# Performance work log

Measured on AMD Instinct MI355X. Metric: run time of the kernel, lower is better.

The kernel has to match this reference:

```python
import jax, jax.numpy as jnp
import numpy as np

N = 100000
F_IN = 128
HID = 8
HEADS = 8
CLASSES = 40
NEG_SLOPE = 0.2


def gat_conv(x, src, dst, W, a_src, a_dst, bias, heads, out_c):
    # x: [N, F]; W: [F, heads*out_c]; a_src/a_dst: [heads, out_c]; bias: [heads*out_c]
    n = x.shape[0]
    h = (x @ W).reshape(n, heads, out_c)                       # [N, H, C]
    al_src = jnp.sum(h * a_src, axis=-1)                       # [N, H]
    al_dst = jnp.sum(h * a_dst, axis=-1)                       # [N, H]
    e = jax.nn.leaky_relu(al_src[src] + al_dst[dst], NEG_SLOPE)  # [E, H]
    # segment softmax over destination node (PyG softmax over edge_index[1])
    m = jax.ops.segment_max(e, dst, num_segments=n)            # [N, H]
    m = jnp.where(jnp.isfinite(m), m, 0.0)
    ex = jnp.exp(e - m[dst])
    denom = jax.ops.segment_sum(ex, dst, num_segments=n)       # [N, H]
    alpha = ex / denom[dst]                                    # [E, H]
    msg = h[src] * alpha[:, :, None]                           # [E, H, C]
    out = jax.ops.segment_sum(msg, dst, num_segments=n)        # [N, H, C]
    return out.reshape(n, heads * out_c) + bias


def setup_inputs() -> dict:
    key = jax.random.key(0)
    ks = jax.random.split(key, 12)
    E = 1600000
    x = jax.random.normal(ks[0], (N, F_IN), dtype=jnp.float32)
    edge_index = jax.random.randint(ks[1], (2, E), 0, N, dtype=jnp.int32)
    # layer 1: in=F_IN, out=HID, heads=HEADS, concat -> 64 channels
    s1 = 1.0 / np.sqrt(F_IN)
    W1 = jax.random.uniform(ks[2], (F_IN, HEADS * HID), jnp.float32, -s1, s1)
    a_src1 = jax.random.uniform(ks[3], (HEADS, HID), jnp.float32, -0.3, 0.3)
    a_dst1 = jax.random.uniform(ks[4], (HEADS, HID), jnp.float32, -0.3, 0.3)
    b1 = jnp.zeros((HEADS * HID,), jnp.float32)
    # layer 2: in=64, out=CLASSES, heads=1
    d2 = HEADS * HID
    s2 = 1.0 / np.sqrt(d2)
    W2 = jax.random.uniform(ks[5], (d2, CLASSES), jnp.float32, -s2, s2)
    a_src2 = jax.random.uniform(ks[6], (1, CLASSES), jnp.float32, -0.3, 0.3)
    a_dst2 = jax.random.uniform(ks[7], (1, CLASSES), jnp.float32, -0.3, 0.3)
    b2 = jnp.zeros((CLASSES,), jnp.float32)
    return {"x": x, "edge_index": edge_index, "W1": W1, "a_src1": a_src1,
            "a_dst1": a_dst1, "b1": b1, "W2": W2, "a_src2": a_src2,
            "a_dst2": a_dst2, "b2": b2}


def reference(x, edge_index, W1, a_src1, a_dst1, b1, W2, a_src2, a_dst2, b2):
    # PyG GATConv adds self-loops by default
    loops = jnp.arange(N, dtype=edge_index.dtype)
    src = jnp.concatenate([edge_index[0], loops])
    dst = jnp.concatenate([edge_index[1], loops])
    h = gat_conv(x, src, dst, W1, a_src1, a_dst1, b1, HEADS, HID)
    h = jax.nn.relu(h)  # dropout is identity in eval mode
    out = gat_conv(h, src, dst, W2, a_src2, a_dst2, b2, 1, CLASSES)
    return jax.nn.log_softmax(out, axis=1)
```

## Files before the change

kernel.cpp:

```cpp
#include <hip/hip_runtime.h>
#include <hip/hip_bf16.h>
#include <math.h>

#define FIN 128
#define HID 8
#define HEADS 8
#define C1 64
#define CLS 40
#define NSLOPE 0.2f
#define NINF (-__builtin_inff())

typedef __hip_bfloat16 bf16;
typedef unsigned int uint32;
typedef int vint4 __attribute__((ext_vector_type(4)));

__device__ __forceinline__ float lrelu(float x) { return x >= 0.f ? x : NSLOPE * x; }
__device__ __forceinline__ vint4 ldnt4(const int* p) {
    return __builtin_nontemporal_load((const vint4*)p);
}
__device__ __forceinline__ float bfLO(uint32 u) { return __uint_as_float(u << 16); }
__device__ __forceinline__ float bfHI(uint32 u) { return __uint_as_float(u & 0xffff0000u); }
__device__ __forceinline__ uint32 packbf(float a, float b) {
    union { bf16 h[2]; uint32 u; } p;
    p.h[0] = __float2bfloat16(a); p.h[1] = __float2bfloat16(b);
    return p.u;
}

__global__ __launch_bounds__(256) void k_scan1(const int* __restrict__ deg,
    int* __restrict__ rowstart, int* __restrict__ bsum, int n) {
    __shared__ int sm[256];
    int t = threadIdx.x, i = blockIdx.x * 256 + t;
    int v = (i < n) ? deg[i] + 1 : 0;
    sm[t] = v; __syncthreads();
    int x = v;
    for (int off = 1; off < 256; off <<= 1) {
        int tv = (t >= off) ? sm[t - off] : 0;
        __syncthreads();
        x += tv; sm[t] = x; __syncthreads();
    }
    if (i < n) rowstart[i] = x - v;
    if (t == 255) bsum[blockIdx.x] = x;
}

__global__ __launch_bounds__(512) void k_scan2(int* __restrict__ bsum, int nb) {
    __shared__ int sm[512];
    int t = threadIdx.x;
    int v = (t < nb) ? bsum[t] : 0;
    sm[t] = v; __syncthreads();
    int x = v;
    for (int off = 1; off < 512; off <<= 1) {
        int tv = (t >= off) ? sm[t - off] : 0;
        __syncthreads();
        x += tv; sm[t] = x; __syncthreads();
    }
    if (t < nb) bsum[t] = x - v;
}

__global__ void k_scan3(int* __restrict__ rowstart, const int* __restrict__ bsum,
                        int n, int total) {
    int i = blockIdx.x * blockDim.x + threadIdx.x;
    if (i < n) rowstart[i] += bsum[i >> 8];
    if (i == 0) rowstart[n] = total;
}

__global__ __launch_bounds__(256) void k_scatter(const int* __restrict__ ei,
    int E, int En, int n, int* __restrict__ rowcur, int* __restrict__ csr) {
    int g = blockIdx.x & 7;
    int per8 = (n + 7) >> 3;
    int lo = g * per8, hi = min(n, lo + per8);
    int idx = (blockIdx.x >> 3) * 256 + threadIdx.x;
    int e0 = idx * 4;
    if (e0 + 3 < E) {
        vint4 dv = ldnt4(ei + E + e0);
        vint4 sv = ldnt4(ei + e0);
        if (dv.x >= lo && dv.x < hi) csr[atomicAdd(&rowcur[dv.x], 1)] = sv.x;
        if (dv.y >= lo && dv.y < hi) csr[atomicAdd(&rowcur[dv.y], 1)] = sv.y;
        if (dv.z >= lo && dv.z < hi) csr[atomicAdd(&rowcur[dv.z], 1)] = sv.z;
        if (dv.w >= lo && dv.w < hi) csr[atomicAdd(&rowcur[dv.w], 1)] = sv.w;
    } else {
        int e_end = min(e0 + 4, En);
        for (int e = e0; e < e_end; ++e) {
            int s, d;
            if (e < E) { s = ei[e]; d = ei[E + e]; } else { s = d = e - E; }
            if (d >= lo && d < hi) csr[atomicAdd(&rowcur[d], 1)] = s;
        }
    }
}

__global__ __launch_bounds__(256) void gemm1_kernel(
    const float* __restrict__ x, const float* __restrict__ W1,
    const float* __restrict__ a_src, const float* __restrict__ a_dst,
    bf16* __restrict__ h1b, float* __restrict__ alS, float* __restrict__ alD,
    int n, const int* __restrict__ ei, int E, int* __restrict__ deg) {
    __shared__ uint32 Wlu[FIN][C1 / 2];
    __shared__ float xs[64][FIN + 4];
    int t = threadIdx.x;
    const float4* W4 = (const float4*)W1;
    for (int i = t; i < FIN * (C1 / 4); i += 256) {
        float4 w = W4[i];
        int row = i / (C1 / 4), c4 = i % (C1 / 4);
        Wlu[row][c4 * 2]     = packbf(w.x, w.y);
        Wlu[row][c4 * 2 + 1] = packbf(w.z, w.w);
    }
    int node0 = blockIdx.x * 64;
    for (int i = t; i < 64 * (FIN / 4); i += 256) {
        int r = i / (FIN / 4), c = i % (FIN / 4);
        int nn = node0 + r;
        float4 v = {0.f, 0.f, 0.f, 0.f};
        if (nn < n) v = ((const float4*)x)[(size_t)nn * (FIN / 4) + c];
        *(float4*)&xs[r][c * 4] = v;
    }
    __syncthreads();
    int cg = t & 15, ng = t >> 4;
    int head = cg >> 1, hc = (cg & 1) * 4;
    float acc[4][4];
    #pragma unroll
    for (int i = 0; i < 4; ++i)
        for (int j = 0; j < 4; ++j) acc[i][j] = 0.f;
    #pragma unroll 2
    for (int k = 0; k < FIN; ++k) {
        uint2 wu = *(const uint2*)&Wlu[k][cg * 2];
        float w0 = bfLO(wu.x), w1 = bfHI(wu.x);
        float w2 = bfLO(wu.y), w3 = bfHI(wu.y);
        #pragma unroll
        for (int i = 0; i < 4; ++i) {
            float xv = xs[ng * 4 + i][k];
            acc[i][0] += xv * w0; acc[i][1] += xv * w1;
            acc[i][2] += xv * w2; acc[i][3] += xv * w3;
        }
    }
    float a_s[4], a_d[4];
    #pragma unroll
    for (int j = 0; j < 4; ++j) {
        a_s[j] = a_src[head * HID + hc + j];
        a_d[j] = a_dst[head * HID + hc + j];
    }
    #pragma unroll
    for (int i = 0; i < 4; ++i) {
        int node = node0 + ng * 4 + i;
        float as = acc[i][0] * a_s[0] + acc[i][1] * a_s[1]
                 + acc[i][2] * a_s[2] + acc[i][3] * a_s[3];
        float ad = acc[i][0] * a_d[0] + acc[i][1] * a_d[1]
                 + acc[i][2] * a_d[2] + acc[i][3] * a_d[3];
        as += __shfl_xor(as, 1, 64);
        ad += __shfl_xor(ad, 1, 64);
        if (node < n) {
            union { ushort4 u; bf16 b[4]; } pk;
            #pragma unroll
            for (int j = 0; j < 4; ++j) pk.b[j] = __float2bfloat16(acc[i][j]);
            ((ushort4*)h1b)[(size_t)node * (C1 / 4) + cg] = pk.u;
            if ((cg & 1) == 0) {
                alS[node * HEADS + head] = as;
                alD[node * HEADS + head] = ad;
            }
        }
    }
    int g = blockIdx.x * 256 + t;
    int gstride = gridDim.x * 256;
    int nI4 = E >> 2;
    for (int idx = g; idx < nI4; idx += gstride) {
        vint4 dv = ldnt4(ei + E + idx * 4);
        atomicAdd(&deg[dv.x], 1); atomicAdd(&deg[dv.y], 1);
        atomicAdd(&deg[dv.z], 1); atomicAdd(&deg[dv.w], 1);
    }
    if (g == 0)
        for (int e = nI4 * 4; e < E; ++e) atomicAdd(&deg[ei[E + e]], 1);
}

__global__ __launch_bounds__(256) void k_agg1(
    const int* __restrict__ csr, const int* __restrict__ rowend,
    const int* __restrict__ deg,
    const float* __restrict__ alS, const float* __restrict__ alD,
    const bf16* __restrict__ h1b, const float* __restrict__ b1,
    const float* __restrict__ W2, const float* __restrict__ aS2,
    const float* __restrict__ aD2,
    bf16* __restrict__ h2b, float* __restrict__ alS2, float* __restrict__ alD2,
    int n) {
    __shared__ int    ls[4][64];
    __shared__ float4 lp4[4][128];
    __shared__ float  xrow[4][64];
    __shared__ float  Wl[C1][CLS];
    int t = threadIdx.x;
    for (int i = t; i < C1 * CLS; i += 256) Wl[i / CLS][i % CLS] = W2[i];
    __syncthreads();
    int lane = t & 63, wv = t >> 6;
    int c32 = lane & 31;
    int par = lane >> 5;
    int hp  = c32 >> 2;
    const float* lpf = (const float*)&lp4[wv][0];
    const uint32* h1u = (const uint32*)h1b;
    int stride = gridDim.x * 4;

    for (int d = blockIdx.x * 4 + wv; d < n; d += stride) {
        float4 ad0 = *(const float4*)(alD + d * HEADS);
        float4 ad1 = *(const float4*)(alD + d * HEADS + 4);
        float adh[8] = {ad0.x, ad0.y, ad0.z, ad0.w, ad1.x, ad1.y, ad1.z, ad1.w};
        int cnt  = deg[d] + 1;
        int base = rowend[d] - cnt;
        float accx = 0.f, accy = 0.f, den = 0.f;
        for (int jb = 0; jb < cnt; jb += 64) {
            int ec = min(64, cnt - jb);
            int jj = jb + lane;
            bool on = jj < cnt;
            int s = on ? csr[base + jj] : 0;
            ls[wv][lane] = s;
            float4 a0 = *(const float4*)(alS + s * HEADS);
            float4 a1 = *(const float4*)(alS + s * HEADS + 4);
            float av[8] = {a0.x, a0.y, a0.z, a0.w, a1.x, a1.y, a1.z, a1.w};
            float pv[8];
            #pragma unroll
            for (int h = 0; h < 8; ++h)
                pv[h] = on ? __expf(lrelu(av[h] + adh[h])) : 0.f;
            lp4[wv][lane * 2]     = make_float4(pv[0], pv[1], pv[2], pv[3]);
            lp4[wv][lane * 2 + 1] = make_float4(pv[4], pv[5], pv[6], pv[7]);
            int j = 0;
            for (; j + 8 <= ec; j += 8) {
                int j0 = j + par, j1 = j + 2 + par, j2 = j + 4 + par, j3 = j + 6 + par;
                int s0 = ls[wv][j0], s1 = ls[wv][j1];
                int s2 = ls[wv][j2], s3 = ls[wv][j3];
                float p0 = lpf[j0 * 8 + hp], p1 = lpf[j1 * 8 + hp];
                float p2 = lpf[j2 * 8 + hp], p3 = lpf[j3 * 8 + hp];
                uint32 u0 = h1u[s0 * 32 + c32], u1 = h1u[s1 * 32 + c32];
                uint32 u2 = h1u[s2 * 32 + c32], u3 = h1u[s3 * 32 + c32];
                accx = fmaf(p0, bfLO(u0), accx); accy = fmaf(p0, bfHI(u0), accy);
                accx = fmaf(p1, bfLO(u1), accx); accy = fmaf(p1, bfHI(u1), accy);
                accx = fmaf(p2, bfLO(u2), accx); accy = fmaf(p2, bfHI(u2), accy);
                accx = fmaf(p3, bfLO(u3), accx); accy = fmaf(p3, bfHI(u3), accy);
                den += p0 + p1 + p2 + p3;
            }
            for (; j < ec; j += 2) {
                int j0 = j + par;
                int s0 = ls[wv][j0];
                float p0 = lpf[j0 * 8 + hp];
                uint32 u0 = h1u[s0 * 32 + c32];
                accx = fmaf(p0, bfLO(u0), accx);
                accy = fmaf(p0, bfHI(u0), accy);
                den += p0;
            }
        }
        accx += __shfl_xor(accx, 32, 64);
        accy += __shfl_xor(accy, 32, 64);
        den  += __shfl_xor(den, 32, 64);
        if (lane < 32) {
            float2 bb = *(const float2*)(b1 + 2 * c32);
            float vx = accx / den + bb.x;
            float vy = accy / den + bb.y;
            vx = vx > 0.f ? vx : 0.f;
            vy = vy > 0.f ? vy : 0.f;
            *(float2*)&xrow[wv][2 * c32] = make_float2(vx, vy);
        }
        bool act = lane < CLS;
        float h2c = 0.f;
        if (act) {
            #pragma unroll 8
            for (int k = 0; k < C1; ++k) h2c = fmaf(xrow[wv][k], Wl[k][lane], h2c);
        }
        float as2 = act ? h2c * aS2[lane] : 0.f;
        float ad2 = act ? h2c * aD2[lane] : 0.f;
        #pragma unroll
        for (int off = 1; off < 64; off <<= 1) {
            as2 += __shfl_xor(as2, off, 64);
            ad2 += __shfl_xor(ad2, off, 64);
        }
        if (act) h2b[d * CLS + lane] = __float2bfloat16(h2c);
        if (lane == 0) { alS2[d] = as2; alD2[d] = ad2; }
    }
}

__global__ __launch_bounds__(256) void k_agg2(
    const int* __restrict__ csr, const int* __restrict__ rowend,
    const int* __restrict__ deg,
    const float* __restrict__ alS, const float* __restrict__ alD,
    const bf16* __restrict__ h2b, const float* __restrict__ b2,
    float* __restrict__ out, int n) {
    __shared__ int2 lsp[4][64];
    int lane = threadIdx.x & 63, wv = threadIdx.x >> 6;
    int d = blockIdx.x * 4 + wv;
    if (d >= n) return;
    int c32 = lane & 31;
    int par = lane >> 5;
    bool actB = c32 < (CLS / 2);
    const uint32* h2u = (const uint32*)h2b;
    float ad = alD[d];
    int cnt  = deg[d] + 1;
    int base = rowend[d] - cnt;
    float accx = 0.f, accy = 0.f, den = 0.f;
    for (int jb = 0; jb < cnt; jb += 64) {
        int ec = min(64, cnt - jb);
        int jj = jb + lane;
        bool on = jj < cnt;
        int s = on ? csr[base + jj] : 0;
        float p = on ? __expf(lrelu(alS[s] + ad)) : 0.f;
        den += p;
        lsp[wv][lane] = make_int2(s, __float_as_int(p));
        if (actB) {
            int j = 0;
            for (; j + 8 <= ec; j += 8) {
                int2 e0 = lsp[wv][j + par],     e1 = lsp[wv][j + 2 + par];
                int2 e2 = lsp[wv][j + 4 + par], e3 = lsp[wv][j + 6 + par];
                uint32 u0 = h2u[e0.x * 20 + c32], u1 = h2u[e1.x * 20 + c32];
                uint32 u2 = h2u[e2.x * 20 + c32], u3 = h2u[e3.x * 20 + c32];
                float p0 = __int_as_float(e0.y), p1 = __int_as_float(e1.y);
                float p2 = __int_as_float(e2.y), p3 = __int_as_float(e3.y);
                accx = fmaf(p0, bfLO(u0), accx); accy = fmaf(p0, bfHI(u0), accy);
                accx = fmaf(p1, bfLO(u1), accx); accy = fmaf(p1, bfHI(u1), accy);
                accx = fmaf(p2, bfLO(u2), accx); accy = fmaf(p2, bfHI(u2), accy);
                accx = fmaf(p3, bfLO(u3), accx); accy = fmaf(p3, bfHI(u3), accy);
            }
            for (; j < ec; j += 2) {
                int2 e0 = lsp[wv][j + par];
                uint32 u0 = h2u[e0.x * 20 + c32];
                float p0 = __int_as_float(e0.y);
                accx = fmaf(p0, bfLO(u0), accx);
                accy = fmaf(p0, bfHI(u0), accy);
            }
        }
    }
    #pragma unroll
    for (int off = 1; off < 64; off <<= 1) den += __shfl_xor(den, off, 64);
    accx += __shfl_xor(accx, 32, 64);
    accy += __shfl_xor(accy, 32, 64);
    bool owner = (lane < 32) && actB;
    float vx = 0.f, vy = 0.f;
    if (owner) {
        float2 bb = *(const float2*)(b2 + 2 * c32);
        vx = accx / den + bb.x;
        vy = accy / den + bb.y;
    }
    float mx = owner ? fmaxf(vx, vy) : NINF;
    #pragma unroll
    for (int off = 1; off < 64; off <<= 1) mx = fmaxf(mx, __shfl_xor(mx, off, 64));
    float sum = owner ? (__expf(vx - mx) + __expf(vy - mx)) : 0.f;
    #pragma unroll
    for (int off = 1; off < 64; off <<= 1) sum += __shfl_xor(sum, off, 64);
    float lse = mx + __logf(sum);
    if (owner)
        *(float2*)(out + (size_t)d * CLS + 2 * c32) = make_float2(vx - lse, vy - lse);
}

extern "C" void kernel_launch(void* const* d_in, const int* in_sizes, int n_in,
                              void* d_out, int out_size, void* d_ws, size_t ws_size,
                              hipStream_t stream) {
    const float* x   = (const float*)d_in[0];
    const int*   ei  = (const int*)d_in[1];
    const float* W1  = (const float*)d_in[2];
    const float* aS1 = (const float*)d_in[3];
    const float* aD1 = (const float*)d_in[4];
    const float* b1  = (const float*)d_in[5];
    const float* W2  = (const float*)d_in[6];
    const float* aS2 = (const float*)d_in[7];
    const float* aD2 = (const float*)d_in[8];
    const float* b2  = (const float*)d_in[9];
    float* out = (float*)d_out;

    int n = in_sizes[0] / FIN;
    int E = in_sizes[1] / 2;
    int En = E + n;

    char* wsb = (char*)d_ws;
    bf16*  h1b  = (bf16*)wsb;
    bf16*  h2b  = h1b + (size_t)n * C1;
    float* alS1 = (float*)(h2b + (size_t)n * CLS);
    float* alD1 = alS1 + (size_t)n * HEADS;
    float* alS2 = alD1 + (size_t)n * HEADS;
    float* alD2 = alS2 + n;
    int*   csr  = (int*)(alD2 + n);
    int*   rowstart = csr + En;
    int*   deg  = rowstart + n + 1;
    int*   bsum = deg + n;

    const int T = 256;
    int nb = (n + 255) / 256;

    (void)hipMemsetAsync(deg, 0, (size_t)n * sizeof(int), stream);
    gemm1_kernel<<<(n + 63) / 64, T, 0, stream>>>(x, W1, aS1, aD1, h1b, alS1, alD1,
                                                  n, ei, E, deg);

    k_scan1<<<nb, T, 0, stream>>>(deg, rowstart, bsum, n);
    k_scan2<<<1, 512, 0, stream>>>(bsum, nb);
    k_scan3<<<nb, T, 0, stream>>>(rowstart, bsum, n, En);
    int chunks = (En + 1023) / 1024;
    k_scatter<<<chunks * 8, T, 0, stream>>>(ei, E, En, n, rowstart, csr);

    k_agg1<<<2048, T, 0, stream>>>(csr, rowstart, deg, alS1, alD1, h1b, b1,
                                   W2, aS2, aD2, h2b, alS2, alD2, n);

    k_agg2<<<(n + 3) / 4, T, 0, stream>>>(csr, rowstart, deg, alS2, alD2, h2b, b2, out, n);
}
```

Before: 330.2 us.

## Compute in-degree via per-block LDS histograms over node slices

Replaces the global atomic degree counting, which did one global atomic per edge across all gemm1 blocks, with a sliced LDS histogram. 256 blocks each own one of 16 node slices and scan a sixteenth of the edges, counting into shared memory. They then flush nonzero bins to global with one atomic per bin. The goal is to cut global atomic contention and traffic. In exchange each block reads its edge share and discards most entries, since only about 1/16 fall in its slice. The flush still issues many global atomics, and the shared buffer must be large enough for about 6250 ints.

```diff
diff --git a/kernel.cpp b/kernel.cpp
--- a/kernel.cpp
+++ b/kernel.cpp
@@ -155,16 +155,31 @@
             }
         }
     }
-    int g = blockIdx.x * 256 + t;
-    int gstride = gridDim.x * 256;
-    int nI4 = E >> 2;
-    for (int idx = g; idx < nI4; idx += gstride) {
-        vint4 dv = ldnt4(ei + E + idx * 4);
-        atomicAdd(&deg[dv.x], 1); atomicAdd(&deg[dv.y], 1);
-        atomicAdd(&deg[dv.z], 1); atomicAdd(&deg[dv.w], 1);
-    }
-    if (g == 0)
-        for (int e = nI4 * 4; e < E; ++e) atomicAdd(&deg[ei[E + e]], 1);
+    if (blockIdx.x < 256) {
+        __syncthreads();
+        int* hist = (int*)&xs[0][0];
+        int SLICE = (n + 15) >> 4;
+        int sl = blockIdx.x & 15;
+        int lo = sl * SLICE, hi = min(n, lo + SLICE);
+        int nbin = hi - lo;
+        for (int i = t; i < nbin; i += 256) hist[i] = 0;
+        __syncthreads();
+        int nI4 = E >> 2;
+        for (int idx = (blockIdx.x >> 4) * 256 + t; idx < nI4; idx += 4096) {
+            vint4 dv = ldnt4(ei + E + idx * 4);
+            if (dv.x >= lo && dv.x < hi) atomicAdd(&hist[dv.x - lo], 1);
+            if (dv.y >= lo && dv.y < hi) atomicAdd(&hist[dv.y - lo], 1);
+            if (dv.z >= lo && dv.z < hi) atomicAdd(&hist[dv.z - lo], 1);
+            if (dv.w >= lo && dv.w < hi) atomicAdd(&hist[dv.w - lo], 1);
+        }
+        if (blockIdx.x == 0)
+            for (int e = nI4 * 4 + t; e < E; e += 256) atomicAdd(&deg[ei[E + e]], 1);
+        __syncthreads();
+        for (int i = t; i < nbin; i += 256) {
+            int v = hist[i];
+            if (v) atomicAdd(&deg[lo + i], v);
+        }
+    }
 }
 
 __global__ __launch_bounds__(256) void k_agg1(
@@ -371,10 +386,12 @@
 
     const int T = 256;
     int nb = (n + 255) / 256;
+    int nblocks = (n + 63) / 64;
+    if (nblocks < 256) nblocks = 256;
 
     (void)hipMemsetAsync(deg, 0, (size_t)n * sizeof(int), stream);
-    gemm1_kernel<<<(n + 63) / 64, T, 0, stream>>>(x, W1, aS1, aD1, h1b, alS1, alD1,
-                                                  n, ei, E, deg);
+    gemm1_kernel<<<nblocks, T, 0, stream>>>(x, W1, aS1, aD1, h1b, alS1, alD1,
+                                            n, ei, E, deg);
 
     k_scan1<<<nb, T, 0, stream>>>(deg, rowstart, bsum, n);
     k_scan2<<<1, 512, 0, stream>>>(bsum, nb);
```

Measured after the change: 317.2 us. -3.9%, faster.
